# Kernel tuning notes

Measured on AMD Instinct MI355X. Metric: run time of the kernel, lower is better.

Reference implementation:

```python
import jax, jax.numpy as jnp
import numpy as np


def setup_inputs() -> dict:
    key = jax.random.key(0)
    ks = jax.random.split(key, 7)
    N, E, D_IN, D_OUT = 50000, 800000, 128, 128
    features = jax.random.normal(ks[0], (N, D_IN), dtype=jnp.float32)
    src = jax.random.randint(ks[1], (E,), 0, N, dtype=jnp.int64)
    dst = jax.random.randint(ks[2], (E,), 0, N, dtype=jnp.int64)
    W1 = jax.random.normal(ks[3], (D_OUT, D_IN), dtype=jnp.float32) * (1.0 / np.sqrt(D_IN))
    b1 = jax.random.normal(ks[4], (D_OUT,), dtype=jnp.float32) * 0.01
    W2 = jax.random.normal(ks[5], (1, 2 * D_OUT), dtype=jnp.float32) * (1.0 / np.sqrt(2 * D_OUT))
    b2 = jax.random.normal(ks[6], (1,), dtype=jnp.float32) * 0.01
    return {"features": features, "src": src, "dst": dst,
            "W1": W1, "b1": b1, "W2": W2, "b2": b2}


def reference(features, src, dst, W1, b1, W2, b2):
    # Gather endpoint features per edge: [E, D_in]
    f_src = features[src]
    f_dst = features[dst]
    # Shared linear projection (torch Linear: x @ W.T + b) -> [E, D_out]
    h_src = jnp.einsum('ed,od->eo', f_src, W1) + b1
    h_dst = jnp.einsum('ed,od->eo', f_dst, W1) + b1
    # Concat [diff, sum] -> [E, 2*D_out]; dropout is identity at inference
    e_feats = jnp.concatenate([h_src - h_dst, h_src + h_dst], axis=1)
    # Final linear to scalar per edge, squeeze, tanh -> [E]
    out = jnp.tanh((jnp.einsum('ef,of->eo', e_feats, W2) + b2).squeeze(-1))
    return out
```

## Files before the change

kernel.cpp:

```cpp
#include <hip/hip_runtime.h>
#include <math.h>

#define D 128


__global__ void __launch_bounds__(256) node_fused_kernel(
        const float* __restrict__ W1, const float* __restrict__ b1,
        const float* __restrict__ W2, const float* __restrict__ b2,
        const float* __restrict__ feat, float2* __restrict__ st, int N) {
    __shared__ float uv[2 * D + 2];
    __shared__ float red[2 * D];
    __shared__ float csc[D];
    int tid = threadIdx.x;
    int d = tid & (D - 1);
    int ch = tid >> 7;
    float u = 0.f, v = 0.f;
    int o0 = ch * 64;
    #pragma unroll 16
    for (int k = 0; k < 64; ++k) {
        int o = o0 + k;
        float wa = W2[o];
        float wb = W2[D + o];
        float w1 = W1[o * D + d];
        u += (wa + wb) * w1;
        v += (wb - wa) * w1;
    }
    if (ch == 0) { red[d] = u; red[D + d] = v; csc[d] = 2.f * W2[D + d] * b1[d]; }
    __syncthreads();
    if (ch == 1) {
        uv[2 * d]     = red[d] + u;
        uv[2 * d + 1] = red[D + d] + v;
    }
    if (tid == 0) {
        float cc = b2[0];
        #pragma unroll 16
        for (int o = 0; o < D; ++o) cc += csc[o];
        uv[2 * D] = cc;
    }
    __syncthreads();
    float c = uv[2 * D];

    int lane = tid & 63;
    int half = lane >> 5;
    int l = lane & 31;
    int waveInBlock = tid >> 6;
    int stride = gridDim.x * 8;
    float4 a = ((const float4*)uv)[2 * l];
    float4 b = ((const float4*)uv)[2 * l + 1];
    for (int node = blockIdx.x * 8 + waveInBlock * 2 + half; node < N; node += stride) {
        float4 f = ((const float4*)(feat + (size_t)node * D))[l];
        float s = f.x * a.x + f.y * a.z + f.z * b.x + f.w * b.z;
        float t = f.x * a.y + f.y * a.w + f.z * b.y + f.w * b.w;
        #pragma unroll
        for (int off = 16; off; off >>= 1) {
            s += __shfl_xor(s, off, 64);
            t += __shfl_xor(t, off, 64);
        }
        if (l == 0) st[node] = make_float2(s + c, t);
    }
}

__global__ void edge_kernel(const int* __restrict__ src, const int* __restrict__ dst,
                            const float2* __restrict__ st, float* __restrict__ out, int E) {
    int i = blockIdx.x * blockDim.x + threadIdx.x;
    int e0 = i * 4;
    if (e0 >= E) return;
    if (e0 + 3 < E) {
        int4 si = ((const int4*)src)[i];
        int4 di = ((const int4*)dst)[i];
        float2 a0 = st[si.x], a1 = st[si.y], a2 = st[si.z], a3 = st[si.w];
        float2 b0 = st[di.x], b1v = st[di.y], b2v = st[di.z], b3 = st[di.w];
        float4 r;
        r.x = tanhf(a0.x + b0.y);
        r.y = tanhf(a1.x + b1v.y);
        r.z = tanhf(a2.x + b2v.y);
        r.w = tanhf(a3.x + b3.y);
        ((float4*)out)[i] = r;
    } else {
        for (int e = e0; e < E; ++e)
            out[e] = tanhf(st[src[e]].x + st[dst[e]].y);
    }
}

__global__ void prep_kernel(const float* __restrict__ W1, const float* __restrict__ b1,
                            const float* __restrict__ W2, const float* __restrict__ b2,
                            float* __restrict__ uvc) {
    __shared__ float su[4 * D];
    __shared__ float sv[4 * D];
    __shared__ float sc[D];
    int tid = threadIdx.x;
    int d = tid & (D - 1);
    int ch = tid >> 7;
    float u = 0.f, v = 0.f;
    int o0 = ch * 32;
    #pragma unroll 8
    for (int k = 0; k < 32; ++k) {
        int o = o0 + k;
        float wa = W2[o];
        float wb = W2[D + o];
        float w1 = W1[o * D + d];
        u += (wa + wb) * w1;
        v += (wb - wa) * w1;
    }
    su[ch * D + d] = u;
    sv[ch * D + d] = v;
    if (ch == 0) sc[d] = 2.f * W2[D + d] * b1[d];
    __syncthreads();
    if (tid < D) {
        uvc[2 * d]     = su[d] + su[D + d] + su[2 * D + d] + su[3 * D + d];
        uvc[2 * d + 1] = sv[d] + sv[D + d] + sv[2 * D + d] + sv[3 * D + d];
    } else if (tid == D) {
        float cc = b2[0];
        for (int o = 0; o < D; ++o) cc += sc[o];
        uvc[2 * D] = cc;
    }
}

__global__ void fused_edge_kernel(const float* __restrict__ feat,
                                  const int* __restrict__ src, const int* __restrict__ dst,
                                  const float* __restrict__ uvc, float* __restrict__ out, int E) {
    int wave = (int)((blockIdx.x * blockDim.x + threadIdx.x) >> 6);
    int lane = threadIdx.x & 63;
    if (wave >= E) return;
    int sn = src[wave], dn = dst[wave];
    float2 fs = ((const float2*)(feat + (size_t)sn * D))[lane];
    float2 fd = ((const float2*)(feat + (size_t)dn * D))[lane];
    float2 p = ((const float2*)uvc)[2 * lane];
    float2 q = ((const float2*)uvc)[2 * lane + 1];
    float acc = fs.x * p.x + fs.y * q.x + fd.x * p.y + fd.y * q.y;
    #pragma unroll
    for (int off = 32; off; off >>= 1) acc += __shfl_xor(acc, off, 64);
    if (lane == 0) out[wave] = tanhf(acc + uvc[2 * D]);
}

extern "C" void kernel_launch(void* const* d_in, const int* in_sizes, int n_in,
                              void* d_out, int out_size, void* d_ws, size_t ws_size,
                              hipStream_t stream) {
    const float* feat = (const float*)d_in[0];
    const int*   src  = (const int*)d_in[1];
    const int*   dst  = (const int*)d_in[2];
    const float* W1   = (const float*)d_in[3];
    const float* b1   = (const float*)d_in[4];
    const float* W2   = (const float*)d_in[5];
    const float* b2   = (const float*)d_in[6];
    float* out = (float*)d_out;

    int N = in_sizes[0] / D;
    int E = in_sizes[1];

    size_t needed = 2 * (size_t)N * sizeof(float);

    if (ws_size >= needed) {
        float2* st = (float2*)d_ws;
        int nblocks = 512;
        if (nblocks > (N + 7) / 8) nblocks = (N + 7) / 8;
        node_fused_kernel<<<nblocks, 256, 0, stream>>>(W1, b1, W2, b2, feat, st, N);
        int nthreads = (E + 3) / 4;
        edge_kernel<<<(nthreads + 255) / 256, 256, 0, stream>>>(src, dst, st, out, E);
    } else {
        float* uvc = (float*)d_ws;
        prep_kernel<<<1, 512, 0, stream>>>(W1, b1, W2, b2, uvc);
        int nblocks = (E + 3) / 4;
        fused_edge_kernel<<<nblocks, 256, 0, stream>>>(feat, src, dst, uvc, out, E);
    }
}
```

Measured before the change: 98.85 us.

## Compute projection vectors once in block 0 and flag-sync other blocks

```diff
diff --git a/kernel.cpp b/kernel.cpp
--- a/kernel.cpp
+++ b/kernel.cpp
@@ -2,51 +2,64 @@
 #include <math.h>
 
 #define D 128
+#define FLAG_MAGIC 0x13572468u
 
 
 __global__ void __launch_bounds__(256) node_fused_kernel(
         const float* __restrict__ W1, const float* __restrict__ b1,
         const float* __restrict__ W2, const float* __restrict__ b2,
-        const float* __restrict__ feat, float2* __restrict__ st, int N) {
-    __shared__ float uv[2 * D + 2];
-    __shared__ float red[2 * D];
-    __shared__ float csc[D];
+        const float* __restrict__ feat, float* __restrict__ uvc,
+        unsigned int* __restrict__ flag, float2* __restrict__ st, int N) {
     int tid = threadIdx.x;
-    int d = tid & (D - 1);
-    int ch = tid >> 7;
-    float u = 0.f, v = 0.f;
-    int o0 = ch * 64;
-    #pragma unroll 16
-    for (int k = 0; k < 64; ++k) {
-        int o = o0 + k;
-        float wa = W2[o];
-        float wb = W2[D + o];
-        float w1 = W1[o * D + d];
-        u += (wa + wb) * w1;
-        v += (wb - wa) * w1;
+    if (blockIdx.x == 0) {
+        __shared__ float red[2 * D];
+        __shared__ float csc[D];
+        int d = tid & (D - 1);
+        int ch = tid >> 7;
+        float u = 0.f, v = 0.f;
+        int o0 = ch * 64;
+        #pragma unroll 16
+        for (int k = 0; k < 64; ++k) {
+            int o = o0 + k;
+            float wa = W2[o];
+            float wb = W2[D + o];
+            float w1 = W1[o * D + d];
+            u += (wa + wb) * w1;
+            v += (wb - wa) * w1;
+        }
+        if (ch == 0) { red[d] = u; red[D + d] = v; csc[d] = 2.f * W2[D + d] * b1[d]; }
+        __syncthreads();
+        if (ch == 1) {
+            uvc[2 * d]     = red[d] + u;
+            uvc[2 * d + 1] = red[D + d] + v;
+        }
+        if (tid == 0) {
+            float cc = b2[0];
+            #pragma unroll
+            for (int o = 0; o < D; ++o) cc += csc[o];
+            uvc[2 * D] = cc;
+        }
+        __threadfence();
+        __syncthreads();
+        if (tid == 0)
+            __hip_atomic_store(flag, FLAG_MAGIC, __ATOMIC_RELEASE, __HIP_MEMORY_SCOPE_AGENT);
+    } else {
+        if (tid == 0) {
+            while (__hip_atomic_load(flag, __ATOMIC_ACQUIRE, __HIP_MEMORY_SCOPE_AGENT)
+                   != FLAG_MAGIC)
+                __builtin_amdgcn_s_sleep(1);
+        }
+        __syncthreads();
     }
-    if (ch == 0) { red[d] = u; red[D + d] = v; csc[d] = 2.f * W2[D + d] * b1[d]; }
-    __syncthreads();
-    if (ch == 1) {
-        uv[2 * d]     = red[d] + u;
-        uv[2 * d + 1] = red[D + d] + v;
-    }
-    if (tid == 0) {
-        float cc = b2[0];
-        #pragma unroll 16
-        for (int o = 0; o < D; ++o) cc += csc[o];
-        uv[2 * D] = cc;
-    }
-    __syncthreads();
-    float c = uv[2 * D];
 
     int lane = tid & 63;
     int half = lane >> 5;
     int l = lane & 31;
     int waveInBlock = tid >> 6;
+    float4 a = ((const float4*)uvc)[2 * l];
+    float4 b = ((const float4*)uvc)[2 * l + 1];
+    float c = uvc[2 * D];
     int stride = gridDim.x * 8;
-    float4 a = ((const float4*)uv)[2 * l];
-    float4 b = ((const float4*)uv)[2 * l + 1];
     for (int node = blockIdx.x * 8 + waveInBlock * 2 + half; node < N; node += stride) {
         float4 f = ((const float4*)(feat + (size_t)node * D))[l];
         float s = f.x * a.x + f.y * a.z + f.z * b.x + f.w * b.z;
@@ -85,16 +98,16 @@
 __global__ void prep_kernel(const float* __restrict__ W1, const float* __restrict__ b1,
                             const float* __restrict__ W2, const float* __restrict__ b2,
                             float* __restrict__ uvc) {
-    __shared__ float su[4 * D];
-    __shared__ float sv[4 * D];
+    __shared__ float su[8 * D];
+    __shared__ float sv[8 * D];
     __shared__ float sc[D];
     int tid = threadIdx.x;
     int d = tid & (D - 1);
     int ch = tid >> 7;
     float u = 0.f, v = 0.f;
-    int o0 = ch * 32;
-    #pragma unroll 8
-    for (int k = 0; k < 32; ++k) {
+    int o0 = ch * 16;
+    #pragma unroll
+    for (int k = 0; k < 16; ++k) {
         int o = o0 + k;
         float wa = W2[o];
         float wb = W2[D + o];
@@ -107,10 +120,14 @@
     if (ch == 0) sc[d] = 2.f * W2[D + d] * b1[d];
     __syncthreads();
     if (tid < D) {
-        uvc[2 * d]     = su[d] + su[D + d] + su[2 * D + d] + su[3 * D + d];
-        uvc[2 * d + 1] = sv[d] + sv[D + d] + sv[2 * D + d] + sv[3 * D + d];
+        float uu = 0.f, vv = 0.f;
+        #pragma unroll
+        for (int j = 0; j < 8; ++j) { uu += su[j * D + d]; vv += sv[j * D + d]; }
+        uvc[2 * d]     = uu;
+        uvc[2 * d + 1] = vv;
     } else if (tid == D) {
         float cc = b2[0];
+        #pragma unroll
         for (int o = 0; o < D; ++o) cc += sc[o];
         uvc[2 * D] = cc;
     }
@@ -148,18 +165,20 @@
     int N = in_sizes[0] / D;
     int E = in_sizes[1];
 
-    size_t needed = 2 * (size_t)N * sizeof(float);
+    float* uvc = (float*)d_ws;
+    unsigned int* flag = (unsigned int*)((float*)d_ws + 512);
+    float2* st = (float2*)((float*)d_ws + 640);
+    size_t needed = (640 + 2 * (size_t)N) * sizeof(float);
 
     if (ws_size >= needed) {
-        float2* st = (float2*)d_ws;
         int nblocks = 512;
-        if (nblocks > (N + 7) / 8) nblocks = (N + 7) / 8;
-        node_fused_kernel<<<nblocks, 256, 0, stream>>>(W1, b1, W2, b2, feat, st, N);
+        int maxb = (N + 7) / 8;
+        if (nblocks > maxb) nblocks = maxb;
+        node_fused_kernel<<<nblocks, 256, 0, stream>>>(W1, b1, W2, b2, feat, uvc, flag, st, N);
         int nthreads = (E + 3) / 4;
         edge_kernel<<<(nthreads + 255) / 256, 256, 0, stream>>>(src, dst, st, out, E);
     } else {
-        float* uvc = (float*)d_ws;
-        prep_kernel<<<1, 512, 0, stream>>>(W1, b1, W2, b2, uvc);
+        prep_kernel<<<1, 1024, 0, stream>>>(W1, b1, W2, b2, uvc);
         int nblocks = (E + 3) / 4;
         fused_edge_kernel<<<nblocks, 256, 0, stream>>>(feat, src, dst, uvc, out, E);
     }
```

Result: slower. 145.1 us (+46.8%).
